# Optimization experiments

Hardware: AMD Instinct MI355X
Metric: run time of the kernel (lower is better)

Reference implementation:

```python
import jax, jax.numpy as jnp
import numpy as np

CORE_DIM = 128
MEMORY_SLOTS = 64
B, S = 4, 4096


def setup_inputs() -> dict:
    key = jax.random.key(0)
    k1, k2, k3, k4, k5 = jax.random.split(key, 5)
    x = jax.random.normal(k1, (B, S, CORE_DIM), dtype=jnp.float32)
    memory_keys = jax.random.normal(k2, (MEMORY_SLOTS, CORE_DIM), dtype=jnp.float32)
    memory_ops = jax.random.normal(k3, (MEMORY_SLOTS, CORE_DIM, CORE_DIM), dtype=jnp.float32)
    # nn.Linear(core_dim, core_dim): weight [out, in], bias [out]
    bound = 1.0 / np.sqrt(CORE_DIM)
    Wq = jax.random.uniform(k4, (CORE_DIM, CORE_DIM), minval=-bound, maxval=bound, dtype=jnp.float32)
    bq = jax.random.uniform(k5, (CORE_DIM,), minval=-bound, maxval=bound, dtype=jnp.float32)
    return {"input_tensor": x, "memory_keys": memory_keys, "memory_ops": memory_ops, "Wq": Wq, "bq": bq}


def reference(input_tensor, memory_keys, memory_ops, Wq, bq):
    dim = input_tensor.shape[-1]
    # query projection: x @ Wq^T + bq
    queries = jnp.einsum('bsd,ed->bse', input_tensor, Wq) + bq
    # soft attention over memory slots
    attn_logits = jnp.einsum('bsd,md->bsm', queries, memory_keys)
    attn_weights = jax.nn.softmax(attn_logits / jnp.sqrt(jnp.float32(dim)), axis=-1)
    # fused: (sum_m attn[bsm] * ops[m]) @ x[bs]  == sum_m attn[bsm] * (ops[m] @ x[bs])
    processed = jnp.einsum('bsm,mde,bse->bsd', attn_weights, memory_ops, input_tensor)
    return processed
```

## Files before the change

### kernel.cpp

```cpp
#include <hip/hip_runtime.h>

typedef __bf16 bf16x8 __attribute__((ext_vector_type(8)));
typedef float f32x4 __attribute__((ext_vector_type(4)));
typedef unsigned int uint4v __attribute__((ext_vector_type(4)));
typedef unsigned short ushort_t;
typedef unsigned int uint_t;

#define RS 0.08838834764831845f

__device__ __forceinline__ ushort_t f2bf(float f) {
    uint_t u = __float_as_uint(f);
    u += 0x7FFFu + ((u >> 16) & 1u);
    return (ushort_t)(u >> 16);
}
__device__ __forceinline__ uint_t pack2(float a, float b) {
    return (uint_t)f2bf(a) | ((uint_t)f2bf(b) << 16);
}
union U4B8 { uint4v u; bf16x8 b; };
__device__ __forceinline__ bf16x8 as_bf(uint4v u) { U4B8 x; x.u = u; return x.b; }

__device__ __forceinline__ int xfrag(int f, int lane) {
    return f * 1072 + ((lane >> 4) * 272) + ((lane & 15) * 16);
}

__global__ __launch_bounds__(256) void prep_kernel(
    const float* __restrict__ ops, const float* __restrict__ keys,
    const float* __restrict__ Wq, const float* __restrict__ bq,
    uint4v* __restrict__ ops_sw, ushort_t* __restrict__ kp_sw,
    float* __restrict__ cb)
{
    const int tid = threadIdx.x;
    const int b = blockIdx.x;
    if (b >= 64) {
        int g = (b - 64) * 256 + tid;
        int L = g & 63, dt = (g >> 6) & 7, ks = (g >> 9) & 3, m = g >> 11;
        int d = dt * 16 + (L & 15);
        int e0 = ks * 32 + ((L >> 4) << 3);
        const float4* s = (const float4*)(ops + (((size_t)(m * 128 + d)) << 7) + e0);
        float4 v0 = s[0], v1 = s[1];
        uint4v o = { pack2(v0.x, v0.y), pack2(v0.z, v0.w),
                     pack2(v1.x, v1.y), pack2(v1.z, v1.w) };
        ops_sw[g] = o;
    } else {
        __shared__ float red[256];
        const int m = b;
        const int d = tid & 127, eh = tid >> 7;
        const float* kr = keys + m * 128 + eh * 64;
        const float* wc = Wq + (size_t)(eh * 64) * 128 + d;
        float acc = 0.f;
        #pragma unroll 8
        for (int e = 0; e < 64; ++e)
            acc = fmaf(kr[e], wc[(size_t)e * 128], acc);
        red[tid] = acc;
        __syncthreads();
        if (tid < 128) {
            float v = red[tid] + red[tid + 128];
            int ki = d >> 5, qq = (d >> 3) & 3, j = d & 7;
            kp_sw[((((ki * 4 + (m >> 4)) * 64) + (qq * 16 + (m & 15))) << 3) | j] = f2bf(v);
        } else if (tid >= 192) {
            int lane = tid - 192;
            float p = keys[m * 128 + lane] * bq[lane]
                    + keys[m * 128 + 64 + lane] * bq[64 + lane];
            #pragma unroll
            for (int off = 1; off < 64; off <<= 1) p += __shfl_xor(p, off);
            if (lane == 0) cb[m] = p;
        }
    }
}

__global__ __launch_bounds__(256, 2) void main_kernel(
    const float* __restrict__ x, const float* __restrict__ cb,
    const ushort_t* __restrict__ kp_sw, const uint4v* __restrict__ ops_sw,
    float* __restrict__ out)
{
    __shared__ __align__(16) unsigned char xs[17152];
    __shared__ float attn_f[32 * 68];

    const int tid = threadIdx.x;
    const int lane = tid & 63;
    const int w = tid >> 6;
    const int q = lane >> 4;
    const int l15 = lane & 15;
    const int tb = blockIdx.x >> 1;
    const int kb = blockIdx.x & 1;
    const int t0 = tb * 64;

    {
        const float4* x4 = (const float4*)(x + (size_t)t0 * 128);
        #pragma unroll
        for (int it = 0; it < 4; ++it) {
            int i = it * 256 + tid;
            int t = i >> 4, kc = i & 15;
            float4 a = x4[t * 32 + kc * 2];
            float4 b2 = x4[t * 32 + kc * 2 + 1];
            uint4v o = { pack2(a.x, a.y), pack2(a.z, a.w),
                         pack2(b2.x, b2.y), pack2(b2.z, b2.w) };
            *(uint4v*)(xs + ((t >> 4) * 4 + (kc >> 2)) * 1072
                          + (kc & 3) * 272 + (t & 15) * 16) = o;
        }
    }
    __syncthreads();

    {
        f32x4 L0 = {0,0,0,0}, L1 = {0,0,0,0}, L2 = {0,0,0,0}, L3 = {0,0,0,0};
        const uint4v* kpf = (const uint4v*)kp_sw;
        #pragma unroll
        for (int ki = 0; ki < 4; ++ki) {
            bf16x8 a = *(const bf16x8*)(xs + xfrag(w * 4 + ki, lane));
            L0 = __builtin_amdgcn_mfma_f32_16x16x32_bf16(a, as_bf(kpf[(ki*4+0)*64 + lane]), L0, 0,0,0);
            L1 = __builtin_amdgcn_mfma_f32_16x16x32_bf16(a, as_bf(kpf[(ki*4+1)*64 + lane]), L1, 0,0,0);
            L2 = __builtin_amdgcn_mfma_f32_16x16x32_bf16(a, as_bf(kpf[(ki*4+2)*64 + lane]), L2, 0,0,0);
            L3 = __builtin_amdgcn_mfma_f32_16x16x32_bf16(a, as_bf(kpf[(ki*4+3)*64 + lane]), L3, 0,0,0);
        }
        float c0 = cb[l15], c1 = cb[16 + l15], c2 = cb[32 + l15], c3 = cb[48 + l15];
        #pragma unroll
        for (int r = 0; r < 4; ++r) {
            float v0 = (L0[r] + c0) * RS;
            float v1 = (L1[r] + c1) * RS;
            float v2 = (L2[r] + c2) * RS;
            float v3 = (L3[r] + c3) * RS;
            float mx = fmaxf(fmaxf(v0, v1), fmaxf(v2, v3));
            #pragma unroll
            for (int off = 1; off < 16; off <<= 1) mx = fmaxf(mx, __shfl_xor(mx, off));
            float e0 = __expf(v0 - mx), e1 = __expf(v1 - mx),
                  e2 = __expf(v2 - mx), e3 = __expf(v3 - mx);
            float sm = e0 + e1 + e2 + e3;
            #pragma unroll
            for (int off = 1; off < 16; off <<= 1) sm += __shfl_xor(sm, off);
            float inv = 1.0f / sm;
            int t = w * 16 + q * 4 + r;
            float ea = (kb == 0) ? e0 : e2;
            float eb = (kb == 0) ? e1 : e3;
            attn_f[(     l15) * 68 + t] = ea * inv;
            attn_f[(16 + l15) * 68 + t] = eb * inv;
        }
    }

    bf16x8 A[4][4];
    #pragma unroll
    for (int tf = 0; tf < 4; ++tf)
        #pragma unroll
        for (int ki = 0; ki < 4; ++ki)
            A[tf][ki] = *(const bf16x8*)(xs + xfrag(tf * 4 + ki, lane));

    __syncthreads();

    const uint4v* ob0 = ops_sw + (size_t)(kb * 32) * 2048 + (size_t)(w * 2    ) * 64 + lane;
    const uint4v* ob1 = ops_sw + (size_t)(kb * 32) * 2048 + (size_t)(w * 2 + 1) * 64 + lane;
    f32x4 C[4][2] = {};
    uint4v B[2][2][4];
    #pragma unroll
    for (int ki = 0; ki < 4; ++ki) {
        B[0][0][ki] = ob0[ki * 512];
        B[0][1][ki] = ob1[ki * 512];
    }

    #pragma unroll 2
    for (int ml = 0; ml < 32; ++ml) {
        const int cur = ml & 1, nxt = cur ^ 1;
        const size_t off = (size_t)((ml < 31) ? ml + 1 : 31) * 2048;
        #pragma unroll
        for (int ki = 0; ki < 4; ++ki) {
            B[nxt][0][ki] = ob0[off + ki * 512];
            B[nxt][1][ki] = ob1[off + ki * 512];
        }
        f32x4 S[4][2] = {};
        #pragma unroll
        for (int ki = 0; ki < 4; ++ki) {
            bf16x8 b0 = as_bf(B[cur][0][ki]);
            bf16x8 b1 = as_bf(B[cur][1][ki]);
            #pragma unroll
            for (int tf = 0; tf < 4; ++tf) {
                S[tf][0] = __builtin_amdgcn_mfma_f32_16x16x32_bf16(A[tf][ki], b0, S[tf][0], 0,0,0);
                S[tf][1] = __builtin_amdgcn_mfma_f32_16x16x32_bf16(A[tf][ki], b1, S[tf][1], 0,0,0);
            }
        }
        #pragma unroll
        for (int tf = 0; tf < 4; ++tf) {
            f32x4 af = *(const f32x4*)&attn_f[ml * 68 + tf * 16 + q * 4];
            #pragma unroll
            for (int dd = 0; dd < 2; ++dd)
                #pragma unroll
                for (int r = 0; r < 4; ++r)
                    C[tf][dd][r] = fmaf(af[r], S[tf][dd][r], C[tf][dd][r]);
        }
    }

    float* op = out + (size_t)t0 * 128 + w * 32 + l15;
    #pragma unroll
    for (int tf = 0; tf < 4; ++tf)
        #pragma unroll
        for (int dd = 0; dd < 2; ++dd)
            #pragma unroll
            for (int r = 0; r < 4; ++r)
                atomicAdd(&op[(size_t)(tf * 16 + q * 4 + r) * 128 + dd * 16], C[tf][dd][r]);
}

extern "C" void kernel_launch(void* const* d_in, const int* in_sizes, int n_in,
                              void* d_out, int out_size, void* d_ws, size_t ws_size,
                              hipStream_t stream)
{
    const float* x    = (const float*)d_in[0];
    const float* keys = (const float*)d_in[1];
    const float* ops  = (const float*)d_in[2];
    const float* Wq   = (const float*)d_in[3];
    const float* bq   = (const float*)d_in[4];
    float* out = (float*)d_out;

    char* ws = (char*)d_ws;
    uint4v*   ops_sw = (uint4v*)ws;
    ushort_t* kp_sw  = (ushort_t*)(ws + 2097152);
    float*    cb     = (float*)(ws + 2097152 + 16384);

    hipMemsetAsync(d_out, 0, (size_t)out_size * sizeof(float), stream);
    prep_kernel<<<576, 256, 0, stream>>>(ops, keys, Wq, bq, ops_sw, kp_sw, cb);
    main_kernel<<<512, 256, 0, stream>>>(x, cb, kp_sw, ops_sw, out);
}
```

Measured before the change: 118.9 us.

## Double token tile per block and use 2x2 warp tiling for ops reuse

Each block now handles 128 tokens instead of 64, with the four warps arranged 2x2 over tokens and output dims. Each warp holds 64 output dims, so every ops fragment loaded from global memory feeds more MFMAs, halving total ops traffic. Attention weights for the next slot are now prefetched from LDS a step ahead. In exchange it uses more registers and LDS (launch bounds drop to one block per SM) and launches only 256 blocks, which lowers occupancy and the parallelism available to hide latency.

```diff
diff --git a/kernel.cpp b/kernel.cpp
--- a/kernel.cpp
+++ b/kernel.cpp
@@ -7,6 +7,7 @@
 typedef unsigned int uint_t;
 
 #define RS 0.08838834764831845f
+#define APF 132
 
 __device__ __forceinline__ ushort_t f2bf(float f) {
     uint_t u = __float_as_uint(f);
@@ -68,13 +69,13 @@
     }
 }
 
-__global__ __launch_bounds__(256, 2) void main_kernel(
+__global__ __launch_bounds__(256, 1) void main_kernel(
     const float* __restrict__ x, const float* __restrict__ cb,
     const ushort_t* __restrict__ kp_sw, const uint4v* __restrict__ ops_sw,
     float* __restrict__ out)
 {
-    __shared__ __align__(16) unsigned char xs[17152];
-    __shared__ float attn_f[32 * 68];
+    __shared__ __align__(16) unsigned char xs[34304];
+    __shared__ float attn_f[32 * APF];
 
     const int tid = threadIdx.x;
     const int lane = tid & 63;
@@ -83,12 +84,14 @@
     const int l15 = lane & 15;
     const int tb = blockIdx.x >> 1;
     const int kb = blockIdx.x & 1;
-    const int t0 = tb * 64;
+    const int t0 = tb * 128;
+    const int wy = w >> 1;
+    const int wx = w & 1;
 
     {
         const float4* x4 = (const float4*)(x + (size_t)t0 * 128);
         #pragma unroll
-        for (int it = 0; it < 4; ++it) {
+        for (int it = 0; it < 8; ++it) {
             int i = it * 256 + tid;
             int t = i >> 4, kc = i & 15;
             float4 a = x4[t * 32 + kc * 2];
@@ -101,12 +104,14 @@
     }
     __syncthreads();
 
-    {
+    const uint4v* kpf = (const uint4v*)kp_sw;
+    #pragma unroll
+    for (int tg2 = 0; tg2 < 2; ++tg2) {
+        const int tgg = w * 2 + tg2;
         f32x4 L0 = {0,0,0,0}, L1 = {0,0,0,0}, L2 = {0,0,0,0}, L3 = {0,0,0,0};
-        const uint4v* kpf = (const uint4v*)kp_sw;
         #pragma unroll
         for (int ki = 0; ki < 4; ++ki) {
-            bf16x8 a = *(const bf16x8*)(xs + xfrag(w * 4 + ki, lane));
+            bf16x8 a = *(const bf16x8*)(xs + xfrag(tgg * 4 + ki, lane));
             L0 = __builtin_amdgcn_mfma_f32_16x16x32_bf16(a, as_bf(kpf[(ki*4+0)*64 + lane]), L0, 0,0,0);
             L1 = __builtin_amdgcn_mfma_f32_16x16x32_bf16(a, as_bf(kpf[(ki*4+1)*64 + lane]), L1, 0,0,0);
             L2 = __builtin_amdgcn_mfma_f32_16x16x32_bf16(a, as_bf(kpf[(ki*4+2)*64 + lane]), L2, 0,0,0);
@@ -128,11 +133,11 @@
             #pragma unroll
             for (int off = 1; off < 16; off <<= 1) sm += __shfl_xor(sm, off);
             float inv = 1.0f / sm;
-            int t = w * 16 + q * 4 + r;
+            int t = tgg * 16 + q * 4 + r;
             float ea = (kb == 0) ? e0 : e2;
             float eb = (kb == 0) ? e1 : e3;
-            attn_f[(     l15) * 68 + t] = ea * inv;
-            attn_f[(16 + l15) * 68 + t] = eb * inv;
+            attn_f[(     l15) * APF + t] = ea * inv;
+            attn_f[(16 + l15) * APF + t] = eb * inv;
         }
     }
 
@@ -141,59 +146,71 @@
     for (int tf = 0; tf < 4; ++tf)
         #pragma unroll
         for (int ki = 0; ki < 4; ++ki)
-            A[tf][ki] = *(const bf16x8*)(xs + xfrag(tf * 4 + ki, lane));
+            A[tf][ki] = *(const bf16x8*)(xs + xfrag((wy * 4 + tf) * 4 + ki, lane));
 
     __syncthreads();
 
-    const uint4v* ob0 = ops_sw + (size_t)(kb * 32) * 2048 + (size_t)(w * 2    ) * 64 + lane;
-    const uint4v* ob1 = ops_sw + (size_t)(kb * 32) * 2048 + (size_t)(w * 2 + 1) * 64 + lane;
-    f32x4 C[4][2] = {};
-    uint4v B[2][2][4];
-    #pragma unroll
-    for (int ki = 0; ki < 4; ++ki) {
-        B[0][0][ki] = ob0[ki * 512];
-        B[0][1][ki] = ob1[ki * 512];
-    }
+    const uint4v* ob = ops_sw + (size_t)(kb * 32) * 2048 + (size_t)(wx * 4) * 64 + lane;
+    f32x4 C[4][4] = {};
+    uint4v B[2][4][4];
+    #pragma unroll
+    for (int ki = 0; ki < 4; ++ki)
+        #pragma unroll
+        for (int df = 0; df < 4; ++df)
+            B[0][ki][df] = ob[ki * 512 + df * 64];
+
+    f32x4 afr[4];
+    #pragma unroll
+    for (int tf = 0; tf < 4; ++tf)
+        afr[tf] = *(const f32x4*)&attn_f[wy * 64 + tf * 16 + q * 4];
 
     #pragma unroll 2
     for (int ml = 0; ml < 32; ++ml) {
         const int cur = ml & 1, nxt = cur ^ 1;
-        const size_t off = (size_t)((ml < 31) ? ml + 1 : 31) * 2048;
-        #pragma unroll
-        for (int ki = 0; ki < 4; ++ki) {
-            B[nxt][0][ki] = ob0[off + ki * 512];
-            B[nxt][1][ki] = ob1[off + ki * 512];
-        }
-        f32x4 S[4][2] = {};
-        #pragma unroll
-        for (int ki = 0; ki < 4; ++ki) {
-            bf16x8 b0 = as_bf(B[cur][0][ki]);
-            bf16x8 b1 = as_bf(B[cur][1][ki]);
-            #pragma unroll
-            for (int tf = 0; tf < 4; ++tf) {
-                S[tf][0] = __builtin_amdgcn_mfma_f32_16x16x32_bf16(A[tf][ki], b0, S[tf][0], 0,0,0);
-                S[tf][1] = __builtin_amdgcn_mfma_f32_16x16x32_bf16(A[tf][ki], b1, S[tf][1], 0,0,0);
+        const size_t moff = (size_t)((ml < 31) ? ml + 1 : 31) * 2048;
+        #pragma unroll
+        for (int ki = 0; ki < 4; ++ki)
+            #pragma unroll
+            for (int df = 0; df < 4; ++df)
+                B[nxt][ki][df] = ob[moff + ki * 512 + df * 64];
+
+        f32x4 afn[4];
+        {
+            const int mn = (ml < 31) ? ml + 1 : 31;
+            #pragma unroll
+            for (int tf = 0; tf < 4; ++tf)
+                afn[tf] = *(const f32x4*)&attn_f[mn * APF + wy * 64 + tf * 16 + q * 4];
+        }
+
+        f32x4 S[4][4] = {};
+        #pragma unroll
+        for (int ki = 0; ki < 4; ++ki)
+            #pragma unroll
+            for (int df = 0; df < 4; ++df) {
+                bf16x8 bfrag = as_bf(B[cur][ki][df]);
+                #pragma unroll
+                for (int tf = 0; tf < 4; ++tf)
+                    S[tf][df] = __builtin_amdgcn_mfma_f32_16x16x32_bf16(A[tf][ki], bfrag, S[tf][df], 0,0,0);
             }
-        }
-        #pragma unroll
-        for (int tf = 0; tf < 4; ++tf) {
-            f32x4 af = *(const f32x4*)&attn_f[ml * 68 + tf * 16 + q * 4];
-            #pragma unroll
-            for (int dd = 0; dd < 2; ++dd)
+        #pragma unroll
+        for (int tf = 0; tf < 4; ++tf)
+            #pragma unroll
+            for (int df = 0; df < 4; ++df)
                 #pragma unroll
                 for (int r = 0; r < 4; ++r)
-                    C[tf][dd][r] = fmaf(af[r], S[tf][dd][r], C[tf][dd][r]);
-        }
-    }
-
-    float* op = out + (size_t)t0 * 128 + w * 32 + l15;
+                    C[tf][df][r] = fmaf(afr[tf][r], S[tf][df][r], C[tf][df][r]);
+        #pragma unroll
+        for (int tf = 0; tf < 4; ++tf) afr[tf] = afn[tf];
+    }
+
+    float* op = out + (size_t)(t0 + wy * 64) * 128 + wx * 64 + l15;
     #pragma unroll
     for (int tf = 0; tf < 4; ++tf)
         #pragma unroll
-        for (int dd = 0; dd < 2; ++dd)
+        for (int df = 0; df < 4; ++df)
             #pragma unroll
             for (int r = 0; r < 4; ++r)
-                atomicAdd(&op[(size_t)(tf * 16 + q * 4 + r) * 128 + dd * 16], C[tf][dd][r]);
+                atomicAdd(&op[(size_t)(tf * 16 + q * 4 + r) * 128 + df * 16], C[tf][df][r]);
 }
 
 extern "C" void kernel_launch(void* const* d_in, const int* in_sizes, int n_in,
@@ -214,5 +231,5 @@
 
     hipMemsetAsync(d_out, 0, (size_t)out_size * sizeof(float), stream);
     prep_kernel<<<576, 256, 0, stream>>>(ops, keys, Wq, bq, ops_sw, kp_sw, cb);
-    main_kernel<<<512, 256, 0, stream>>>(x, cb, kp_sw, ops_sw, out);
-}
+    main_kernel<<<256, 256, 0, stream>>>(x, cb, kp_sw, ops_sw, out);
+}
```

After: 157.1 us. 32.1% more time.
